# Optimization experiments

Measured on AMD Instinct MI355X. Metric: run time of the kernel, lower is better.

The kernel has to match this reference:

```python
import jax, jax.numpy as jnp
import numpy as np
import math

D_MODEL = 64
N_HEADS = 4
D_HEAD = D_MODEL // N_HEADS
SCALE = math.sqrt(D_HEAD)
B, NQ, NK = 32, 16384, 31


def setup_inputs() -> dict:
    key = jax.random.key(0)
    kq, kk, kv, km, kw, kb = jax.random.split(key, 6)
    Q = jax.random.normal(kq, (B, NQ, D_MODEL), dtype=jnp.float32)
    K = jax.random.normal(kk, (B, NK, D_MODEL), dtype=jnp.float32)
    V = jax.random.normal(kv, (B, NK, D_MODEL), dtype=jnp.float32)
    mask = jax.random.randint(km, (B, NK), 0, 2).astype(jnp.bool_)
    # out_proj: nn.Linear(d_model, d_model)
    lim = 1.0 / math.sqrt(D_MODEL)
    W_out = jax.random.uniform(kw, (D_MODEL, D_MODEL), minval=-lim, maxval=lim, dtype=jnp.float32)
    b_out = jax.random.uniform(kb, (D_MODEL,), minval=-lim, maxval=lim, dtype=jnp.float32)
    return {"Q": Q, "K": K, "V": V, "mask": mask, "W_out": W_out, "b_out": b_out}


def reference(Q, K, V, mask, W_out, b_out):
    Bn, Nq, D = Q.shape
    Nk = K.shape[1]
    # (B, H, N, d_head)
    q = Q.reshape(Bn, Nq, N_HEADS, D_HEAD).transpose(0, 2, 1, 3)
    k = K.reshape(Bn, Nk, N_HEADS, D_HEAD).transpose(0, 2, 1, 3)
    v = V.reshape(Bn, Nk, N_HEADS, D_HEAD).transpose(0, 2, 1, 3)
    # (B, H, Nq, Nk)
    attn = jnp.einsum('bhqd,bhkd->bhqk', q, k) / SCALE
    attn = jnp.where(mask[:, None, None, :], attn, -jnp.inf)
    attn = jax.nn.softmax(attn, axis=-1)
    attn = jnp.nan_to_num(attn, nan=0.0)
    out = jnp.einsum('bhqk,bhkd->bhqd', attn, v)
    out = out.transpose(0, 2, 1, 3).reshape(Bn, Nq, D)
    return out @ W_out.T + b_out
```

## Files before the change

kernel.cpp:

```cpp
#include <hip/hip_runtime.h>
#include <math.h>

typedef _Float16 half4_t __attribute__((ext_vector_type(4)));
typedef _Float16 half8_t __attribute__((ext_vector_type(8)));
typedef __fp16   fp16x2  __attribute__((ext_vector_type(2)));
typedef float    f32x4   __attribute__((ext_vector_type(4)));

#define B_   32
#define NQ_  16384
#define NK_  31
#define DM_  64
#define BLK_PER_B 64
#define ITERS 4

static __device__ __forceinline__ half4_t cvt4(f32x4 f) {
  fp16x2 lo = __builtin_amdgcn_cvt_pkrtz(f[0], f[1]);
  fp16x2 hi = __builtin_amdgcn_cvt_pkrtz(f[2], f[3]);
  half4_t r;
  r[0] = (_Float16)lo[0]; r[1] = (_Float16)lo[1];
  r[2] = (_Float16)hi[0]; r[3] = (_Float16)hi[1];
  return r;
}

__global__ __launch_bounds__(256) void attn(
    const float* __restrict__ Q, const float* __restrict__ K,
    const float* __restrict__ V, const unsigned char* __restrict__ mraw,
    const float* __restrict__ W, const float* __restrict__ bout,
    float* __restrict__ out) {
  int b    = blockIdx.x >> 6;
  int blk  = blockIdx.x & 63;
  int tid  = threadIdx.x;
  int wave = tid >> 6, lane = tid & 63;
  int lq = lane & 15, quad = lane >> 4;

  __shared__ half8_t lds_kf[4][64];
  __shared__ half8_t lds_vw[8][2][64];

  const f32x4 fzero = {0.f, 0.f, 0.f, 0.f};

  unsigned mb;
  {
    unsigned char c0 = 0, c1 = 0;
    if (lane < 62) { c0 = mraw[2 * lane]; c1 = mraw[2 * lane + 1]; }
    unsigned long long m3f =
        __ballot(lane < 62 && (c0 == 0x3f || c1 == 0x3f));
    unsigned long long moff =
        __ballot(lane < 62 && ((((2 * lane) & 3) != 0 && c0 != 0) || c1 != 0));
    int mode = m3f ? 2 : (moff ? 0 : 1);
    int nz = 0;
    if (lane < NK_) {
      int idx = b * NK_ + lane;
      nz = (mode == 0) ? (mraw[idx] != 0)
         : (mode == 1) ? (((const int*)mraw)[idx] != 0)
                       : (((const float*)mraw)[idx] != 0.0f);
    }
    mb = (unsigned)__ballot(nz) & 0x7fffffffu;
  }

  f32x4 cbias[2];
  #pragma unroll
  for (int tt = 0; tt < 2; ++tt)
    #pragma unroll
    for (int r = 0; r < 4; ++r) {
      int key = 16 * tt + 4 * quad + r;
      cbias[tt][r] = ((mb >> key) & 1u) ? 0.0f : -1e30f;
    }

  #pragma unroll
  for (int j = 0; j < 2; ++j) {
    int f  = wave * 2 + j;
    int tt = f >> 2, h = f & 3;
    int k  = 16 * tt + lq;
    f32x4 fv = fzero;
    if (k < NK_)
      fv = *(const f32x4*)(K + ((size_t)b * NK_ + k) * DM_ + 16 * h + 4 * quad);
    ((half4_t*)&lds_kf[h][lane])[tt] = cvt4(fv * 0.25f);
  }

  {
    half4_t af[8];
    #pragma unroll
    for (int s = 0; s < 8; ++s) {
      int k = 16 * (s & 1) + lq, h = s >> 1;
      f32x4 f = fzero;
      if (k < NK_)
        f = *(const f32x4*)(V + ((size_t)b * NK_ + k) * DM_ + 16 * h + 4 * quad);
      af[s] = cvt4(f);
    }
    half4_t bf[4];
    #pragma unroll
    for (int h = 0; h < 4; ++h) {
      f32x4 f = *(const f32x4*)(W + (16 * wave + lq) * DM_ + 16 * h + 4 * quad);
      bf[h] = cvt4(f);
    }
    #pragma unroll
    for (int s = 0; s < 8; ++s) {
      f32x4 m = __builtin_amdgcn_mfma_f32_16x16x16f16(af[s], bf[s >> 1],
                                                      fzero, 0, 0, 0);
      ((half4_t*)&lds_vw[s][wave >> 1][lane])[wave & 1] = cvt4(m);
    }
  }

  f32x4 bias[4];
  #pragma unroll
  for (int dt = 0; dt < 4; ++dt)
    bias[dt] = *(const f32x4*)(bout + 16 * dt + 4 * quad);

  __syncthreads();

  int w = blk * 4 + wave;
  const float* qrow = Q + ((size_t)b * NQ_ + lq) * DM_ + 4 * quad;

  f32x4 qraw[4];
  #pragma unroll
  for (int h = 0; h < 4; ++h)
    qraw[h] = *(const f32x4*)(qrow + (size_t)(w * 16) * DM_ + 16 * h);

  #pragma unroll 1
  for (int it = 0; it < ITERS; ++it) {
    int q0 = (w + it * 256) * 16;

    f32x4 qnext[4];
    if (it < ITERS - 1) {
      #pragma unroll
      for (int h = 0; h < 4; ++h)
        qnext[h] = *(const f32x4*)(qrow + (size_t)(q0 + 4096) * DM_ + 16 * h);
    }

    half4_t qf[4];
    #pragma unroll
    for (int h = 0; h < 4; ++h) qf[h] = cvt4(qraw[h]);

    half4_t pf[8];
    #pragma unroll
    for (int h = 0; h < 4; ++h) {
      half8_t kk = lds_kf[h][lane];
      half4_t k0 = __builtin_shufflevector(kk, kk, 0, 1, 2, 3);
      half4_t k1 = __builtin_shufflevector(kk, kk, 4, 5, 6, 7);
      f32x4 c0 = __builtin_amdgcn_mfma_f32_16x16x16f16(k0, qf[h], cbias[0], 0, 0, 0);
      f32x4 c1 = __builtin_amdgcn_mfma_f32_16x16x16f16(k1, qf[h], cbias[1], 0, 0, 0);
      f32x4 e0, e1;
      #pragma unroll
      for (int r = 0; r < 4; ++r) { e0[r] = __expf(c0[r]); e1[r] = __expf(c1[r]); }
      float sum = (e0[0] + e0[1]) + (e0[2] + e0[3]) +
                  (e1[0] + e1[1]) + (e1[2] + e1[3]);
      sum += __shfl_xor(sum, 16);
      sum += __shfl_xor(sum, 32);
      float inv = (sum > 0.f) ? __builtin_amdgcn_rcpf(sum) : 0.f;
      pf[2 * h + 0] = cvt4(e0 * inv);
      pf[2 * h + 1] = cvt4(e1 * inv);
    }

    f32x4 acc[4] = {fzero, fzero, fzero, fzero};
    #pragma unroll
    for (int s = 0; s < 8; ++s) {
      half8_t v01 = lds_vw[s][0][lane];
      half8_t v23 = lds_vw[s][1][lane];
      half4_t a0 = __builtin_shufflevector(v01, v01, 0, 1, 2, 3);
      half4_t a1 = __builtin_shufflevector(v01, v01, 4, 5, 6, 7);
      half4_t a2 = __builtin_shufflevector(v23, v23, 0, 1, 2, 3);
      half4_t a3 = __builtin_shufflevector(v23, v23, 4, 5, 6, 7);
      acc[0] = __builtin_amdgcn_mfma_f32_16x16x16f16(a0, pf[s], acc[0], 0, 0, 0);
      acc[1] = __builtin_amdgcn_mfma_f32_16x16x16f16(a1, pf[s], acc[1], 0, 0, 0);
      acc[2] = __builtin_amdgcn_mfma_f32_16x16x16f16(a2, pf[s], acc[2], 0, 0, 0);
      acc[3] = __builtin_amdgcn_mfma_f32_16x16x16f16(a3, pf[s], acc[3], 0, 0, 0);
    }

    float* obase = out + ((size_t)b * NQ_ + q0 + lq) * DM_ + 4 * quad;
    #pragma unroll
    for (int dt = 0; dt < 4; ++dt)
      *(f32x4*)(obase + 16 * dt) = acc[dt] + bias[dt];

    if (it < ITERS - 1) {
      #pragma unroll
      for (int h = 0; h < 4; ++h) qraw[h] = qnext[h];
    }
  }
}

extern "C" void kernel_launch(void* const* d_in, const int* in_sizes, int n_in,
                              void* d_out, int out_size, void* d_ws, size_t ws_size,
                              hipStream_t stream) {
  const float*         Q    = (const float*)d_in[0];
  const float*         K    = (const float*)d_in[1];
  const float*         V    = (const float*)d_in[2];
  const unsigned char* mask = (const unsigned char*)d_in[3];
  const float*         W    = (const float*)d_in[4];
  const float*         bo   = (const float*)d_in[5];
  float*               out  = (float*)d_out;

  hipLaunchKernelGGL(attn, dim3(B_ * BLK_PER_B), dim3(256), 0, stream,
                     Q, K, V, mask, W, bo, out);
}
```

Before: 248.9 us.

## Software-pipeline softmax and PV GEMM across tiles, use exp2 and nontemporal stores

Hoists the first Q load above the mask and K/V/W setup so it overlaps with that prologue. Restructures the loop into a software pipeline where the softmax of the next tile is computed before the PV GEMM and store of the previous tile. Folds log2(e) into the K scale so the native exp2 instruction replaces __expf. Output stores become nontemporal to avoid polluting cache. The fully unrolled pipeline raises register pressure and may lower occupancy.

```diff
diff --git a/kernel.cpp b/kernel.cpp
--- a/kernel.cpp
+++ b/kernel.cpp
@@ -12,6 +12,7 @@
 #define DM_  64
 #define BLK_PER_B 64
 #define ITERS 4
+#define KSCALE 0.3606738222635048f
 
 static __device__ __forceinline__ half4_t cvt4(f32x4 f) {
   fp16x2 lo = __builtin_amdgcn_cvt_pkrtz(f[0], f[1]);
@@ -37,6 +38,14 @@
   __shared__ half8_t lds_vw[8][2][64];
 
   const f32x4 fzero = {0.f, 0.f, 0.f, 0.f};
+
+  int w = blk * 4 + wave;
+  const float* qrow = Q + ((size_t)b * NQ_ + lq) * DM_ + 4 * quad;
+
+  f32x4 qraw[4];
+  #pragma unroll
+  for (int h = 0; h < 4; ++h)
+    qraw[h] = *(const f32x4*)(qrow + (size_t)(w * 16) * DM_ + 16 * h);
 
   unsigned mb;
   {
@@ -74,7 +83,7 @@
     f32x4 fv = fzero;
     if (k < NK_)
       fv = *(const f32x4*)(K + ((size_t)b * NK_ + k) * DM_ + 16 * h + 4 * quad);
-    ((half4_t*)&lds_kf[h][lane])[tt] = cvt4(fv * 0.25f);
+    ((half4_t*)&lds_kf[h][lane])[tt] = cvt4(fv * KSCALE);
   }
 
   {
@@ -108,40 +117,21 @@
 
   __syncthreads();
 
-  int w = blk * 4 + wave;
-  const float* qrow = Q + ((size_t)b * NQ_ + lq) * DM_ + 4 * quad;
-
-  f32x4 qraw[4];
-  #pragma unroll
-  for (int h = 0; h < 4; ++h)
-    qraw[h] = *(const f32x4*)(qrow + (size_t)(w * 16) * DM_ + 16 * h);
-
-  #pragma unroll 1
-  for (int it = 0; it < ITERS; ++it) {
-    int q0 = (w + it * 256) * 16;
-
-    f32x4 qnext[4];
-    if (it < ITERS - 1) {
-      #pragma unroll
-      for (int h = 0; h < 4; ++h)
-        qnext[h] = *(const f32x4*)(qrow + (size_t)(q0 + 4096) * DM_ + 16 * h);
-    }
-
-    half4_t qf[4];
-    #pragma unroll
-    for (int h = 0; h < 4; ++h) qf[h] = cvt4(qraw[h]);
-
-    half4_t pf[8];
+  auto softtile = [&](const f32x4 qr[4], half4_t pf[8]) {
     #pragma unroll
     for (int h = 0; h < 4; ++h) {
       half8_t kk = lds_kf[h][lane];
       half4_t k0 = __builtin_shufflevector(kk, kk, 0, 1, 2, 3);
       half4_t k1 = __builtin_shufflevector(kk, kk, 4, 5, 6, 7);
-      f32x4 c0 = __builtin_amdgcn_mfma_f32_16x16x16f16(k0, qf[h], cbias[0], 0, 0, 0);
-      f32x4 c1 = __builtin_amdgcn_mfma_f32_16x16x16f16(k1, qf[h], cbias[1], 0, 0, 0);
+      half4_t qf = cvt4(qr[h]);
+      f32x4 c0 = __builtin_amdgcn_mfma_f32_16x16x16f16(k0, qf, cbias[0], 0, 0, 0);
+      f32x4 c1 = __builtin_amdgcn_mfma_f32_16x16x16f16(k1, qf, cbias[1], 0, 0, 0);
       f32x4 e0, e1;
       #pragma unroll
-      for (int r = 0; r < 4; ++r) { e0[r] = __expf(c0[r]); e1[r] = __expf(c1[r]); }
+      for (int r = 0; r < 4; ++r) {
+        e0[r] = __builtin_amdgcn_exp2f(c0[r]);
+        e1[r] = __builtin_amdgcn_exp2f(c1[r]);
+      }
       float sum = (e0[0] + e0[1]) + (e0[2] + e0[3]) +
                   (e1[0] + e1[1]) + (e1[2] + e1[3]);
       sum += __shfl_xor(sum, 16);
@@ -150,7 +140,9 @@
       pf[2 * h + 0] = cvt4(e0 * inv);
       pf[2 * h + 1] = cvt4(e1 * inv);
     }
-
+  };
+
+  auto gemm2store = [&](const half4_t pf[8], int q0) {
     f32x4 acc[4] = {fzero, fzero, fzero, fzero};
     #pragma unroll
     for (int s = 0; s < 8; ++s) {
@@ -165,17 +157,38 @@
       acc[2] = __builtin_amdgcn_mfma_f32_16x16x16f16(a2, pf[s], acc[2], 0, 0, 0);
       acc[3] = __builtin_amdgcn_mfma_f32_16x16x16f16(a3, pf[s], acc[3], 0, 0, 0);
     }
-
     float* obase = out + ((size_t)b * NQ_ + q0 + lq) * DM_ + 4 * quad;
     #pragma unroll
-    for (int dt = 0; dt < 4; ++dt)
-      *(f32x4*)(obase + 16 * dt) = acc[dt] + bias[dt];
-
+    for (int dt = 0; dt < 4; ++dt) {
+      f32x4 v = acc[dt] + bias[dt];
+      __builtin_nontemporal_store(v, (f32x4*)(obase + 16 * dt));
+    }
+  };
+
+  f32x4 qnext[4];
+  #pragma unroll
+  for (int h = 0; h < 4; ++h)
+    qnext[h] = *(const f32x4*)(qrow + (size_t)((w + 256) * 16) * DM_ + 16 * h);
+
+  half4_t pfA[8];
+  softtile(qraw, pfA);
+
+  #pragma unroll
+  for (int it = 1; it < ITERS; ++it) {
+    #pragma unroll
+    for (int h = 0; h < 4; ++h) qraw[h] = qnext[h];
     if (it < ITERS - 1) {
       #pragma unroll
-      for (int h = 0; h < 4; ++h) qraw[h] = qnext[h];
-    }
-  }
+      for (int h = 0; h < 4; ++h)
+        qnext[h] = *(const f32x4*)(qrow + (size_t)((w + (it + 1) * 256) * 16) * DM_ + 16 * h);
+    }
+    half4_t pfB[8];
+    softtile(qraw, pfB);
+    gemm2store(pfA, (w + (it - 1) * 256) * 16);
+    #pragma unroll
+    for (int j = 0; j < 8; ++j) pfA[j] = pfB[j];
+  }
+  gemm2store(pfA, (w + (ITERS - 1) * 256) * 16);
 }
 
 extern "C" void kernel_launch(void* const* d_in, const int* in_sizes, int n_in,
```

New measurement: 259.4 us. 1.04x slower.
